# Kernel tuning notes

Measured on AMD Instinct MI355X. Metric: run time of the kernel, lower is better.

Reference implementation:

```python
import jax, jax.numpy as jnp
import numpy as np


def _primes_below(n):
    primes = []
    for i in range(2, n):
        if all(i % p for p in primes):
            primes.append(i)
    return np.array(primes, dtype=np.int32)  # 168 primes for n=1000

_PRIMES = _primes_below(1000)  # shape (168,)


def setup_inputs() -> dict:
    key = jax.random.key(0)
    k1, k2, k3 = jax.random.split(key, 3)
    B, N = 64, 524288
    x = jax.random.normal(k1, (B, N), dtype=jnp.float32)
    kernel = jax.random.normal(k2, (168, 1000), dtype=jnp.float32)
    bias = jax.random.normal(k3, (168, 1000), dtype=jnp.float32)
    return {"x": x, "kernel": kernel, "bias": bias}


def _prime_mask(weights, n):
    # mask[k] = sum_p weights[p, k mod prime_p]; equivalent to the tf.map_fn
    # tile-and-truncate construct in the original layer.
    pos = jnp.arange(n, dtype=jnp.int32)                    # (N,)
    mods = pos[None, :] % jnp.asarray(_PRIMES)[:, None]     # (168, N)
    gathered = jnp.take_along_axis(weights, mods, axis=1)   # (168, N)
    return gathered.sum(axis=0)                             # (N,)


def reference(x, kernel, bias):
    n = x.shape[1]
    w = _prime_mask(kernel, n)  # (N,)
    b = _prime_mask(bias, n)    # (N,)
    # broadcast over batch, same as expand_dims(..., axis=0) in the original
    return x * w[None, :] + b[None, :]
```

## Files before the change

kernel.cpp:

```cpp
#include <hip/hip_runtime.h>
#include <stdint.h>

#define N_COLS 524288
#define N_PRIMES 168
#define BLOCK 256
#define ROW_CHUNKS 8
#define CG_TOTAL (N_COLS / 4)
#define GTHREADS (N_COLS / 4)
#define PCHUNK 21

static constexpr uint32_t PRIMES[N_PRIMES] = {
      2,   3,   5,   7,  11,  13,  17,  19,  23,  29,
     31,  37,  41,  43,  47,  53,  59,  61,  67,  71,
     73,  79,  83,  89,  97, 101, 103, 107, 109, 113,
    127, 131, 137, 139, 149, 151, 157, 163, 167, 173,
    179, 181, 191, 193, 197, 199, 211, 223, 227, 229,
    233, 239, 241, 251, 257, 263, 269, 271, 277, 281,
    283, 293, 307, 311, 313, 317, 331, 337, 347, 349,
    353, 359, 367, 373, 379, 383, 389, 397, 401, 409,
    419, 421, 431, 433, 439, 443, 449, 457, 461, 463,
    467, 479, 487, 491, 499, 503, 509, 521, 523, 541,
    547, 557, 563, 569, 571, 577, 587, 593, 599, 601,
    607, 613, 617, 619, 631, 641, 643, 647, 653, 659,
    661, 673, 677, 683, 691, 701, 709, 719, 727, 733,
    739, 743, 751, 757, 761, 769, 773, 787, 797, 809,
    811, 821, 823, 827, 829, 839, 853, 857, 859, 863,
    877, 881, 883, 887, 907, 911, 919, 929, 937, 941,
    947, 953, 967, 971, 977, 983, 991, 997
};

__global__ __launch_bounds__(BLOCK) void bwl_zero_ws(float4* __restrict__ ws)
{
    const int g = blockIdx.x * BLOCK + threadIdx.x;
    ws[g] = make_float4(0.f, 0.f, 0.f, 0.f);
}

template <int I0>
__device__ __forceinline__ void accum21(uint32_t g,
                                        const float* __restrict__ kern,
                                        const float* __restrict__ bias,
                                        float* w, float* b)
{
#pragma unroll
    for (int j = 0; j < PCHUNK; ++j) {
        const uint32_t p = PRIMES[I0 + j];
        const int off = (I0 + j) * 1000;
        const uint32_t d = GTHREADS % p;
        uint32_t m = g % p;
        w[0] += kern[off + (int)m];  b[0] += bias[off + (int)m];
        m += d; if (m >= p) m -= p;
        w[1] += kern[off + (int)m];  b[1] += bias[off + (int)m];
        m += d; if (m >= p) m -= p;
        w[2] += kern[off + (int)m];  b[2] += bias[off + (int)m];
        m += d; if (m >= p) m -= p;
        w[3] += kern[off + (int)m];  b[3] += bias[off + (int)m];
    }
}

__global__ __launch_bounds__(BLOCK) void bwl_prime_mask(
    const float* __restrict__ kern,
    const float* __restrict__ bias,
    float* __restrict__ wsw,
    float* __restrict__ wsb)
{
    const uint32_t g = blockIdx.x * BLOCK + threadIdx.x;
    float w[4] = {0.f, 0.f, 0.f, 0.f};
    float b[4] = {0.f, 0.f, 0.f, 0.f};

    switch (blockIdx.y) {
        case 0: accum21<  0>(g, kern, bias, w, b); break;
        case 1: accum21< 21>(g, kern, bias, w, b); break;
        case 2: accum21< 42>(g, kern, bias, w, b); break;
        case 3: accum21< 63>(g, kern, bias, w, b); break;
        case 4: accum21< 84>(g, kern, bias, w, b); break;
        case 5: accum21<105>(g, kern, bias, w, b); break;
        case 6: accum21<126>(g, kern, bias, w, b); break;
        default: accum21<147>(g, kern, bias, w, b); break;
    }

#pragma unroll
    for (int q = 0; q < 4; ++q) {
        atomicAdd(&wsw[g + q * GTHREADS], w[q]);
        atomicAdd(&wsb[g + q * GTHREADS], b[q]);
    }
}

__global__ __launch_bounds__(BLOCK) void bwl_prime_stream(
    const float* __restrict__ x,
    const float4* __restrict__ wsw,
    const float4* __restrict__ wsb,
    float* __restrict__ out)
{
    const int cg = blockIdx.x * BLOCK + threadIdx.x;
    const int r0 = blockIdx.y * (64 / ROW_CHUNKS);

    const float4 w = wsw[cg];
    const float4 b = wsb[cg];

    const float4* __restrict__ x4 = (const float4*)x;
    float4* __restrict__ o4 = (float4*)out;

#pragma unroll
    for (int i = 0; i < 64 / ROW_CHUNKS; ++i) {
        const size_t off = (size_t)(r0 + i) * CG_TOTAL + cg;
        float4 xv = x4[off];
        float4 ov;
        ov.x = fmaf(xv.x, w.x, b.x);
        ov.y = fmaf(xv.y, w.y, b.y);
        ov.z = fmaf(xv.z, w.z, b.z);
        ov.w = fmaf(xv.w, w.w, b.w);
        o4[off] = ov;
    }
}

__global__ __launch_bounds__(BLOCK) void bwl_prime_fused(
    const float* __restrict__ x,
    const float* __restrict__ kern,
    const float* __restrict__ bias,
    float* __restrict__ out,
    int B)
{
    const int tid  = blockIdx.x * BLOCK + threadIdx.x;
    const uint32_t col0 = (uint32_t)tid * 4;

    float w0 = 0.f, w1 = 0.f, w2 = 0.f, w3 = 0.f;
    float b0 = 0.f, b1 = 0.f, b2 = 0.f, b3 = 0.f;
#pragma unroll
    for (int i = 0; i < N_PRIMES; ++i) {
        const uint32_t p = PRIMES[i];
        const int rowoff = i * 1000;
        uint32_t m0 = col0 % p;
        uint32_t m1 = m0 + 1; if (m1 == p) m1 = 0;
        uint32_t m2 = m1 + 1; if (m2 == p) m2 = 0;
        uint32_t m3 = m2 + 1; if (m3 == p) m3 = 0;
        w0 += kern[rowoff + (int)m0];  b0 += bias[rowoff + (int)m0];
        w1 += kern[rowoff + (int)m1];  b1 += bias[rowoff + (int)m1];
        w2 += kern[rowoff + (int)m2];  b2 += bias[rowoff + (int)m2];
        w3 += kern[rowoff + (int)m3];  b3 += bias[rowoff + (int)m3];
    }

    const float4* __restrict__ x4 = (const float4*)x;
    float4* __restrict__ o4 = (float4*)out;
#pragma unroll 4
    for (int r = 0; r < B; ++r) {
        const size_t off = (size_t)r * CG_TOTAL + tid;
        float4 xv = x4[off];
        float4 ov;
        ov.x = fmaf(xv.x, w0, b0);
        ov.y = fmaf(xv.y, w1, b1);
        ov.z = fmaf(xv.z, w2, b2);
        ov.w = fmaf(xv.w, w3, b3);
        o4[off] = ov;
    }
}

extern "C" void kernel_launch(void* const* d_in, const int* in_sizes, int n_in,
                              void* d_out, int out_size, void* d_ws, size_t ws_size,
                              hipStream_t stream) {
    const float* x    = (const float*)d_in[0];
    const float* kern = (const float*)d_in[1];
    const float* bias = (const float*)d_in[2];
    float* out = (float*)d_out;

    const int B = in_sizes[0] / N_COLS;
    const size_t need = (size_t)2 * N_COLS * sizeof(float);

    if (ws_size >= need) {
        float* wsw = (float*)d_ws;
        float* wsb = wsw + N_COLS;

        bwl_zero_ws<<<(2 * N_COLS / 4) / BLOCK, BLOCK, 0, stream>>>((float4*)d_ws);

        dim3 mgrid(GTHREADS / BLOCK, 8);
        bwl_prime_mask<<<mgrid, BLOCK, 0, stream>>>(kern, bias, wsw, wsb);

        dim3 sgrid(CG_TOTAL / BLOCK, ROW_CHUNKS);
        bwl_prime_stream<<<sgrid, BLOCK, 0, stream>>>(x, (const float4*)wsw,
                                                      (const float4*)wsb, out);
    } else {
        bwl_prime_fused<<<CG_TOTAL / BLOCK, BLOCK, 0, stream>>>(x, kern, bias, out, B);
    }
}
```

Measured before the change: 294.9 us.

## Fuse mask computation and streaming into one kernel with LDS transpose

Replaces the three-kernel workspace pipeline (zero, atomic mask accumulation split over 8 prime chunks, row-chunked stream) with a single fused kernel. Each block computes mask values for 1024 columns, with each thread handling columns strided by 256 so the gathers coalesce. The values are transposed through shared memory to float4 per thread, and then all 64 rows are streamed. This removes the workspace round trip, the atomics and two launches. In exchange the grid drops to 512 blocks, and each thread serially runs all 168 primes before its streaming loop, which reduces parallelism and overlap.

Measured after the change: 267.6 us. -9.3%, faster.

```diff
diff --git a/kernel.cpp b/kernel.cpp
--- a/kernel.cpp
+++ b/kernel.cpp
@@ -2,12 +2,11 @@
 #include <stdint.h>
 
 #define N_COLS 524288
+#define N_ROWS 64
 #define N_PRIMES 168
 #define BLOCK 256
-#define ROW_CHUNKS 8
+#define COLS_PER_BLOCK 1024
 #define CG_TOTAL (N_COLS / 4)
-#define GTHREADS (N_COLS / 4)
-#define PCHUNK 21
 
 static constexpr uint32_t PRIMES[N_PRIMES] = {
       2,   3,   5,   7,  11,  13,  17,  19,  23,  29,
@@ -29,127 +28,58 @@
     947, 953, 967, 971, 977, 983, 991, 997
 };
 
-__global__ __launch_bounds__(BLOCK) void bwl_zero_ws(float4* __restrict__ ws)
-{
-    const int g = blockIdx.x * BLOCK + threadIdx.x;
-    ws[g] = make_float4(0.f, 0.f, 0.f, 0.f);
-}
-
-template <int I0>
-__device__ __forceinline__ void accum21(uint32_t g,
-                                        const float* __restrict__ kern,
-                                        const float* __restrict__ bias,
-                                        float* w, float* b)
-{
-#pragma unroll
-    for (int j = 0; j < PCHUNK; ++j) {
-        const uint32_t p = PRIMES[I0 + j];
-        const int off = (I0 + j) * 1000;
-        const uint32_t d = GTHREADS % p;
-        uint32_t m = g % p;
-        w[0] += kern[off + (int)m];  b[0] += bias[off + (int)m];
-        m += d; if (m >= p) m -= p;
-        w[1] += kern[off + (int)m];  b[1] += bias[off + (int)m];
-        m += d; if (m >= p) m -= p;
-        w[2] += kern[off + (int)m];  b[2] += bias[off + (int)m];
-        m += d; if (m >= p) m -= p;
-        w[3] += kern[off + (int)m];  b[3] += bias[off + (int)m];
-    }
-}
-
-__global__ __launch_bounds__(BLOCK) void bwl_prime_mask(
+__global__ __launch_bounds__(BLOCK) void bwl_prime_fused_v2(
+    const float* __restrict__ x,
     const float* __restrict__ kern,
     const float* __restrict__ bias,
-    float* __restrict__ wsw,
-    float* __restrict__ wsb)
+    float* __restrict__ out)
 {
-    const uint32_t g = blockIdx.x * BLOCK + threadIdx.x;
-    float w[4] = {0.f, 0.f, 0.f, 0.f};
-    float b[4] = {0.f, 0.f, 0.f, 0.f};
+    __shared__ float wl[COLS_PER_BLOCK];
+    __shared__ float bl[COLS_PER_BLOCK];
 
-    switch (blockIdx.y) {
-        case 0: accum21<  0>(g, kern, bias, w, b); break;
-        case 1: accum21< 21>(g, kern, bias, w, b); break;
-        case 2: accum21< 42>(g, kern, bias, w, b); break;
-        case 3: accum21< 63>(g, kern, bias, w, b); break;
-        case 4: accum21< 84>(g, kern, bias, w, b); break;
-        case 5: accum21<105>(g, kern, bias, w, b); break;
-        case 6: accum21<126>(g, kern, bias, w, b); break;
-        default: accum21<147>(g, kern, bias, w, b); break;
+    const int t = threadIdx.x;
+    const uint32_t col0 = (uint32_t)blockIdx.x * COLS_PER_BLOCK + (uint32_t)t;
+
+    float w0 = 0.f, w1 = 0.f, w2 = 0.f, w3 = 0.f;
+    float b0 = 0.f, b1 = 0.f, b2 = 0.f, b3 = 0.f;
+
+#pragma unroll
+    for (int i = 0; i < N_PRIMES; ++i) {
+        const uint32_t p = PRIMES[i];
+        const int off = i * 1000;
+        const uint32_t d = 256u % p;
+        uint32_t m = col0 % p;
+        w0 += kern[off + (int)m];  b0 += bias[off + (int)m];
+        m += d; if (m >= p) m -= p;
+        w1 += kern[off + (int)m];  b1 += bias[off + (int)m];
+        m += d; if (m >= p) m -= p;
+        w2 += kern[off + (int)m];  b2 += bias[off + (int)m];
+        m += d; if (m >= p) m -= p;
+        w3 += kern[off + (int)m];  b3 += bias[off + (int)m];
     }
 
-#pragma unroll
-    for (int q = 0; q < 4; ++q) {
-        atomicAdd(&wsw[g + q * GTHREADS], w[q]);
-        atomicAdd(&wsb[g + q * GTHREADS], b[q]);
-    }
-}
+    wl[t]       = w0;  bl[t]       = b0;
+    wl[t + 256] = w1;  bl[t + 256] = b1;
+    wl[t + 512] = w2;  bl[t + 512] = b2;
+    wl[t + 768] = w3;  bl[t + 768] = b3;
+    __syncthreads();
 
-__global__ __launch_bounds__(BLOCK) void bwl_prime_stream(
-    const float* __restrict__ x,
-    const float4* __restrict__ wsw,
-    const float4* __restrict__ wsb,
-    float* __restrict__ out)
-{
-    const int cg = blockIdx.x * BLOCK + threadIdx.x;
-    const int r0 = blockIdx.y * (64 / ROW_CHUNKS);
+    const float4 wv = ((const float4*)wl)[t];
+    const float4 bv = ((const float4*)bl)[t];
 
-    const float4 w = wsw[cg];
-    const float4 b = wsb[cg];
-
+    const int cg = blockIdx.x * BLOCK + t;
     const float4* __restrict__ x4 = (const float4*)x;
     float4* __restrict__ o4 = (float4*)out;
 
-#pragma unroll
-    for (int i = 0; i < 64 / ROW_CHUNKS; ++i) {
-        const size_t off = (size_t)(r0 + i) * CG_TOTAL + cg;
+#pragma unroll 8
+    for (int r = 0; r < N_ROWS; ++r) {
+        const size_t off = (size_t)r * CG_TOTAL + cg;
         float4 xv = x4[off];
         float4 ov;
-        ov.x = fmaf(xv.x, w.x, b.x);
-        ov.y = fmaf(xv.y, w.y, b.y);
-        ov.z = fmaf(xv.z, w.z, b.z);
-        ov.w = fmaf(xv.w, w.w, b.w);
-        o4[off] = ov;
-    }
-}
-
-__global__ __launch_bounds__(BLOCK) void bwl_prime_fused(
-    const float* __restrict__ x,
-    const float* __restrict__ kern,
-    const float* __restrict__ bias,
-    float* __restrict__ out,
-    int B)
-{
-    const int tid  = blockIdx.x * BLOCK + threadIdx.x;
-    const uint32_t col0 = (uint32_t)tid * 4;
-
-    float w0 = 0.f, w1 = 0.f, w2 = 0.f, w3 = 0.f;
-    float b0 = 0.f, b1 = 0.f, b2 = 0.f, b3 = 0.f;
-#pragma unroll
-    for (int i = 0; i < N_PRIMES; ++i) {
-        const uint32_t p = PRIMES[i];
-        const int rowoff = i * 1000;
-        uint32_t m0 = col0 % p;
-        uint32_t m1 = m0 + 1; if (m1 == p) m1 = 0;
-        uint32_t m2 = m1 + 1; if (m2 == p) m2 = 0;
-        uint32_t m3 = m2 + 1; if (m3 == p) m3 = 0;
-        w0 += kern[rowoff + (int)m0];  b0 += bias[rowoff + (int)m0];
-        w1 += kern[rowoff + (int)m1];  b1 += bias[rowoff + (int)m1];
-        w2 += kern[rowoff + (int)m2];  b2 += bias[rowoff + (int)m2];
-        w3 += kern[rowoff + (int)m3];  b3 += bias[rowoff + (int)m3];
-    }
-
-    const float4* __restrict__ x4 = (const float4*)x;
-    float4* __restrict__ o4 = (float4*)out;
-#pragma unroll 4
-    for (int r = 0; r < B; ++r) {
-        const size_t off = (size_t)r * CG_TOTAL + tid;
-        float4 xv = x4[off];
-        float4 ov;
-        ov.x = fmaf(xv.x, w0, b0);
-        ov.y = fmaf(xv.y, w1, b1);
-        ov.z = fmaf(xv.z, w2, b2);
-        ov.w = fmaf(xv.w, w3, b3);
+        ov.x = fmaf(xv.x, wv.x, bv.x);
+        ov.y = fmaf(xv.y, wv.y, bv.y);
+        ov.z = fmaf(xv.z, wv.z, bv.z);
+        ov.w = fmaf(xv.w, wv.w, bv.w);
         o4[off] = ov;
     }
 }
@@ -157,27 +87,12 @@
 extern "C" void kernel_launch(void* const* d_in, const int* in_sizes, int n_in,
                               void* d_out, int out_size, void* d_ws, size_t ws_size,
                               hipStream_t stream) {
+    (void)in_sizes; (void)n_in; (void)d_ws; (void)ws_size;
     const float* x    = (const float*)d_in[0];
     const float* kern = (const float*)d_in[1];
     const float* bias = (const float*)d_in[2];
     float* out = (float*)d_out;
 
-    const int B = in_sizes[0] / N_COLS;
-    const size_t need = (size_t)2 * N_COLS * sizeof(float);
-
-    if (ws_size >= need) {
-        float* wsw = (float*)d_ws;
-        float* wsb = wsw + N_COLS;
-
-        bwl_zero_ws<<<(2 * N_COLS / 4) / BLOCK, BLOCK, 0, stream>>>((float4*)d_ws);
-
-        dim3 mgrid(GTHREADS / BLOCK, 8);
-        bwl_prime_mask<<<mgrid, BLOCK, 0, stream>>>(kern, bias, wsw, wsb);
-
-        dim3 sgrid(CG_TOTAL / BLOCK, ROW_CHUNKS);
-        bwl_prime_stream<<<sgrid, BLOCK, 0, stream>>>(x, (const float4*)wsw,
-                                                      (const float4*)wsb, out);
-    } else {
-        bwl_prime_fused<<<CG_TOTAL / BLOCK, BLOCK, 0, stream>>>(x, kern, bias, out, B);
-    }
+    bwl_prime_fused_v2<<<N_COLS / COLS_PER_BLOCK, BLOCK, 0, stream>>>(
+        x, kern, bias, out);
 }
```
